# Optimization experiments

Measured on AMD Instinct MI355X. Metric: run time of the kernel, lower is better.

Reference implementation:

```python
import jax, jax.numpy as jnp
import numpy as np

EPS = 1e-5

def _conv(x, w, pad):
    # NCHW conv, stride 1, no bias
    return jax.lax.conv_general_dilated(x, w, (1, 1), [(pad, pad), (pad, pad)],
                                        dimension_numbers=('NCHW', 'OIHW', 'NCHW'))

def _bn(x, g, b, m, v):
    # inference-mode BatchNorm2d folded to scale/shift
    s = g * jax.lax.rsqrt(v + EPS)
    return x * s[None, :, None, None] + (b - m * s)[None, :, None, None]

def _cbr(x, w, g, b, m, v):
    # convolution helper module: 3x3 conv (pad 1, no bias) + BN + ReLU
    return jax.nn.relu(_bn(_conv(x, w, 1), g, b, m, v))


def setup_inputs() -> dict:
    key = jax.random.key(0)
    ks = iter(jax.random.split(key, 40))
    dim, mid, B, H, W = 256, 128, 4, 128, 128
    def conv_w(shape):
        fan = shape[1] * shape[2] * shape[3]
        return jax.random.normal(next(ks), shape, jnp.float32) / np.float32(np.sqrt(fan))
    def bn_p(c):
        return (jax.random.normal(next(ks), (c,), jnp.float32) * 0.1 + 1.0,
                jax.random.normal(next(ks), (c,), jnp.float32) * 0.1,
                jax.random.normal(next(ks), (c,), jnp.float32) * 0.1,
                jax.random.uniform(next(ks), (c,), jnp.float32, 0.5, 1.5))
    x = jax.random.normal(next(ks), (B, dim, H, W), jnp.float32)
    w_p1 = conv_w((mid, dim, 3, 3)); g_p1, b_p1, m_p1, v_p1 = bn_p(mid)
    w_p2 = conv_w((mid, dim, 3, 3)); g_p2, b_p2, m_p2, v_p2 = bn_p(mid)
    w_pc = conv_w((dim, mid, 3, 3)); g_pb, b_pb, m_pb, v_pb = bn_p(dim)
    w_c1 = conv_w((dim, dim, 1, 1)); g_b1, b_b1, m_b1, v_b1 = bn_p(dim)
    w_c2 = conv_w((dim, dim, 3, 3)); g_c2, b_c2, m_c2, v_c2 = bn_p(dim)
    return dict(x=x,
                w_p1=w_p1, g_p1=g_p1, b_p1=b_p1, m_p1=m_p1, v_p1=v_p1,
                w_p2=w_p2, g_p2=g_p2, b_p2=b_p2, m_p2=m_p2, v_p2=v_p2,
                w_pc=w_pc, g_pb=g_pb, b_pb=b_pb, m_pb=m_pb, v_pb=v_pb,
                w_c1=w_c1, g_b1=g_b1, b_b1=b_b1, m_b1=m_b1, v_b1=v_b1,
                w_c2=w_c2, g_c2=g_c2, b_c2=b_c2, m_c2=m_c2, v_c2=v_c2)


def reference(x, w_p1, g_p1, b_p1, m_p1, v_p1,
              w_p2, g_p2, b_p2, m_p2, v_p2,
              w_pc, g_pb, b_pb, m_pb, v_pb,
              w_c1, g_b1, b_b1, m_b1, v_b1,
              w_c2, g_c2, b_c2, m_c2, v_c2):
    p1 = _cbr(x, w_p1, g_p1, b_p1, m_p1, v_p1)          # [B,128,H,W]
    top = jax.lax.cummax(p1, axis=2, reverse=True)       # TopPool: max over rows below
    p2 = _cbr(x, w_p2, g_p2, b_p2, m_p2, v_p2)          # [B,128,H,W]
    left = jax.lax.cummax(p2, axis=3, reverse=True)      # LeftPool: max over cols to the right
    p_bn1 = _bn(_conv(top + left, w_pc, 1), g_pb, b_pb, m_pb, v_pb)  # [B,dim,H,W]
    bn1 = _bn(_conv(x, w_c1, 0), g_b1, b_b1, m_b1, v_b1)             # 1x1 skip branch
    relu1 = jax.nn.relu(p_bn1 + bn1)
    return _cbr(relu1, w_c2, g_c2, b_c2, m_c2, v_c2)
```

## Files before the change

kernel.cpp:

```cpp
#include <hip/hip_runtime.h>
#include <hip/hip_bf16.h>

#define HH 128
#define WW 128
#define BB 4
#define NPIX 16384
#define EPSV 1e-5f

using bfrag = __attribute__((ext_vector_type(8))) short;
using f32x4 = __attribute__((ext_vector_type(4))) float;
using us8   = __attribute__((ext_vector_type(8))) unsigned short;

__device__ __forceinline__ float bf2f(ushort u) {
  union { unsigned int i; float f; } x; x.i = ((unsigned int)u) << 16; return x.f;
}
__device__ __forceinline__ ushort f2bf(float f) {
  union { float f; unsigned int i; } x; x.f = f;
  unsigned int r = x.i + 0x7fffu + ((x.i >> 16) & 1u);
  return (ushort)(r >> 16);
}

#define GLOAD16(gsrc, ldst) \
  __builtin_amdgcn_global_load_lds( \
      (const __attribute__((address_space(1))) unsigned int*)(gsrc), \
      (__attribute__((address_space(3))) unsigned int*)(ldst), 16, 0, 0)

template<int CIN1, int TAPS1, int CIN2, int TAPS2, int EPI>
__global__ __launch_bounds__(256, 2)
void convgemm(const ushort* __restrict__ B1,
              const ushort* __restrict__ B2,
              const ushort* __restrict__ wR,
              const float*  __restrict__ tb,
              const float*  __restrict__ tb2,
              void*          __restrict__ outp,
              const ushort* __restrict__ zerop)
{
  __shared__ ushort lds[2][16384];
  constexpr int nch1 = CIN1 / 64;
  constexpr int nch2 = (CIN2 > 0) ? CIN2 / 64 : 0;
  constexpr int NCH  = TAPS1 * nch1 + TAPS2 * nch2;

  const int g  = blockIdx.x & 7;
  const int r  = blockIdx.x >> 3;
  const int bo = r >> 4;
  const int h  = g * 16 + (r & 15);
  const int o_base = (bo & 1) * 128;
  const int b  = bo >> 1;

  const int tid  = threadIdx.x;
  const int lane = tid & 63;
  const int wid  = tid >> 6;
  const int m0 = (wid >> 1) * 64;
  const int n0 = (wid & 1) * 64;

  f32x4 acc[4][4];
  #pragma unroll
  for (int i = 0; i < 4; ++i)
    #pragma unroll
    for (int j = 0; j < 4; ++j) acc[i][j] = (f32x4){0.f, 0.f, 0.f, 0.f};

  int rowB[4], ro1[4], ro2[4];
  #pragma unroll
  for (int s = 0; s < 4; ++s) {
    const int boff = (wid * 4 + s) * 1024 + lane * 16;
    rowB[s] = boff >> 7;
    const int sl8 = ((((boff >> 4) & 7) ^ (rowB[s] & 7)) << 3);
    ro1[s] = rowB[s] * CIN1 + sl8;
    ro2[s] = (CIN2 > 0) ? rowB[s] * CIN2 + sl8 : 0;
  }
  const size_t B1base = (size_t)b * NPIX * CIN1;
  const size_t B2base = (CIN2 > 0) ? (size_t)b * NPIX * CIN2 : 0;

  auto stage = [&](int t, int buf) {
    char* base = (char*)&lds[buf][0];
    const ushort* wsrc = wR + ((size_t)t * 256 + o_base) * 64;
    const ushort* bch;
    int zr; bool oob, ph2;
    if (CIN2 == 0 || t < TAPS1 * nch1) {
      const int tap = t / nch1, ch = t - tap * nch1;
      const int dy = (TAPS1 == 9) ? tap / 3 - 1 : 0;
      const int dx = (TAPS1 == 9) ? tap - (tap / 3) * 3 - 1 : 0;
      const int hy = h + dy;
      oob = (hy < 0) | (hy >= HH);
      zr  = (dx < 0) ? 0 : ((dx > 0) ? 127 : -1);
      bch = B1 + B1base + (size_t)(hy * WW + dx) * CIN1 + ch * 64;
      ph2 = false;
    } else {
      const int ch = t - TAPS1 * nch1;
      oob = false; zr = -1;
      bch = B2 + B2base + (size_t)(h * WW) * CIN2 + ch * 64;
      ph2 = true;
    }
    #pragma unroll
    for (int s = 0; s < 4; ++s) {
      const int off = (wid * 4 + s) * 1024;
      GLOAD16((const char*)wsrc + off + lane * 16, base + off);
      const int roff = ph2 ? ro2[s] : ro1[s];
      const ushort* bs = (oob || rowB[s] == zr) ? zerop : (bch + roff);
      GLOAD16(bs, base + 16384 + off);
    }
  };

  auto compute = [&](int buf) {
    const char* base = (const char*)&lds[buf][0];
    bfrag af[2][4], bfv[2][4];
    #pragma unroll
    for (int kc = 0; kc < 2; ++kc) {
      const int sw = ((((kc << 2) | (lane >> 4)) ^ (lane & 7)) << 4);
      #pragma unroll
      for (int mf = 0; mf < 4; ++mf)
        af[kc][mf] = *(const bfrag*)(base + (m0 + mf * 16 + (lane & 15)) * 128 + sw);
      #pragma unroll
      for (int nf = 0; nf < 4; ++nf)
        bfv[kc][nf] = *(const bfrag*)(base + 16384 + (n0 + nf * 16 + (lane & 15)) * 128 + sw);
    }
    __builtin_amdgcn_s_setprio(1);
    #pragma unroll
    for (int kc = 0; kc < 2; ++kc)
      #pragma unroll
      for (int mf = 0; mf < 4; ++mf)
        #pragma unroll
        for (int nf = 0; nf < 4; ++nf)
          acc[mf][nf] = __builtin_amdgcn_mfma_f32_16x16x32_bf16(
              af[kc][mf], bfv[kc][nf], acc[mf][nf], 0, 0, 0);
    __builtin_amdgcn_s_setprio(0);
  };

  stage(0, 0);
  int cur = 0;
  for (int t = 0; t < NCH; ++t) {
    asm volatile("s_waitcnt vmcnt(0)" ::: "memory");
    __builtin_amdgcn_s_barrier();
    __builtin_amdgcn_sched_barrier(0);
    if (t + 1 < NCH) stage(t + 1, cur ^ 1);
    compute(cur);
    cur ^= 1;
  }

  if (EPI == 4) {
    __syncthreads();
    ushort* ct = (ushort*)&lds[0][0];
    const int pl0 = n0 + (lane & 15);
    #pragma unroll
    for (int mf = 0; mf < 4; ++mf) {
      #pragma unroll
      for (int r2 = 0; r2 < 4; ++r2) {
        const int ol = m0 + mf * 16 + (lane >> 4) * 4 + r2;
        const int o  = o_base + ol;
        const float bias = tb[o] + tb2[o];
        #pragma unroll
        for (int nf = 0; nf < 4; ++nf)
          ct[(pl0 + nf * 16) * 136 + ol] =
              f2bf(fmaxf(acc[mf][nf][r2] + bias, 0.f));
      }
    }
    __syncthreads();
    const int p  = tid >> 1;
    const int hf = tid & 1;
    ushort* dst = (ushort*)outp +
                  ((size_t)b * NPIX + h * WW + p) * 256 + o_base + hf * 64;
    const ushort* src = ct + p * 136 + hf * 64;
    #pragma unroll
    for (int j = 0; j < 8; ++j)
      *(us8*)(dst + j * 8) = *(const us8*)(src + j * 8);
    return;
  }

  const int pc0 = h * WW + n0 + (lane & 15);
  #pragma unroll
  for (int mf = 0; mf < 4; ++mf) {
    #pragma unroll
    for (int r2 = 0; r2 < 4; ++r2) {
      const int o = o_base + m0 + mf * 16 + (lane >> 4) * 4 + r2;
      const float bias = tb[o];
      #pragma unroll
      for (int nf = 0; nf < 4; ++nf) {
        const int p = pc0 + nf * 16;
        float v = fmaxf(acc[mf][nf][r2] + bias, 0.f);
        const size_t oi = ((size_t)(b * 256 + o)) * NPIX + p;
        if (EPI == 0) ((ushort*)outp)[oi] = f2bf(v);
        else          ((float*)outp)[oi] = v;
      }
    }
  }
}

struct WSeg {
  const float *W, *g, *bb, *mm, *vv;
  ushort* dst; float* tb;
  int CIN, COUT, TAPS, o_off, cb, start, end;
};

__device__ __forceinline__ void wrepack_one(const WSeg& s, int e) {
  const int tap = e % s.TAPS;
  const int ci  = (e / s.TAPS) % s.CIN;
  const int o   = e / (s.TAPS * s.CIN);
  const int oi  = o + s.o_off;
  const float sc = s.g[o] * rsqrtf(s.vv[o] + EPSV);
  const int nch = s.CIN / 64;
  const int ch = ci >> 6, kl = ci & 63;
  const int slot = (kl >> 3) ^ (oi & 7);
  s.dst[(((size_t)((s.cb + tap * nch + ch) * s.COUT) + oi) << 6) +
        (slot << 3) + (kl & 7)] = f2bf(s.W[e] * sc);
  if (ci == 0 && tap == 0) s.tb[oi] = s.bb[o] - s.mm[o] * sc;
}

__global__ __launch_bounds__(256)
void wrepack_all(WSeg s0, WSeg s1, WSeg s2, WSeg s3, WSeg s4) {
  const int id = blockIdx.x * 256 + threadIdx.x;
  if (id < s0.end)      wrepack_one(s0, id - s0.start);
  else if (id < s1.end) wrepack_one(s1, id - s1.start);
  else if (id < s2.end) wrepack_one(s2, id - s2.start);
  else if (id < s3.end) wrepack_one(s3, id - s3.start);
  else if (id < s4.end) wrepack_one(s4, id - s4.start);
}

__global__ __launch_bounds__(256)
void repack_x(const float* __restrict__ x, ushort* __restrict__ xT)
{
  const int b  = blockIdx.z;
  const int cq = threadIdx.x >> 6;
  const int pg = threadIdx.x & 63;
  const int p0 = blockIdx.x * 256 + pg * 4;
  const size_t xb = (size_t)b * 256 * NPIX;
  ushort* ob = xT + ((size_t)b * NPIX + p0) * 256 + cq * 64;
  for (int cc = 0; cc < 64; cc += 8) {
    us8 v[4];
    #pragma unroll
    for (int j = 0; j < 8; ++j) {
      const float4 q = *(const float4*)&x[xb + (size_t)(cq * 64 + cc + j) * NPIX + p0];
      v[0][j] = f2bf(q.x); v[1][j] = f2bf(q.y);
      v[2][j] = f2bf(q.z); v[3][j] = f2bf(q.w);
    }
    #pragma unroll
    for (int k = 0; k < 4; ++k)
      *(us8*)(ob + (size_t)k * 256 + cc) = v[k];
  }
}

__global__ __launch_bounds__(256)
void scan_top(const ushort* __restrict__ p12T, ushort* __restrict__ topT)
{
  const int b = blockIdx.x >> 6;
  const int w = (blockIdx.x & 63) * 2 + (threadIdx.x >> 7);
  const int c = threadIdx.x & 127;
  const size_t ib = (size_t)b * NPIX;
  float cur = -3.4e38f;
  for (int h8 = HH - 8; h8 >= 0; h8 -= 8) {
    float v[8];
    #pragma unroll
    for (int j = 0; j < 8; ++j)
      v[j] = bf2f(p12T[(ib + (size_t)(h8 + j) * WW + w) * 256 + c]);
    #pragma unroll
    for (int j = 7; j >= 0; --j) {
      cur = fmaxf(cur, v[j]);
      topT[(ib + (size_t)(h8 + j) * WW + w) * 128 + c] = f2bf(cur);
    }
  }
}

__global__ __launch_bounds__(256)
void scan_left_sum(const ushort* __restrict__ p12T,
                   const ushort* __restrict__ topT,
                   ushort* __restrict__ sumT)
{
  const int b = blockIdx.x >> 6;
  const int h = (blockIdx.x & 63) * 2 + (threadIdx.x >> 7);
  const int c = threadIdx.x & 127;
  const size_t ib = (size_t)b * NPIX + (size_t)h * WW;
  float cur = -3.4e38f;
  for (int w8 = WW - 8; w8 >= 0; w8 -= 8) {
    float v[8], tv[8];
    #pragma unroll
    for (int j = 0; j < 8; ++j) {
      v[j]  = bf2f(p12T[(ib + w8 + j) * 256 + 128 + c]);
      tv[j] = bf2f(topT[(ib + w8 + j) * 128 + c]);
    }
    #pragma unroll
    for (int j = 7; j >= 0; --j) {
      cur = fmaxf(cur, v[j]);
      sumT[(ib + w8 + j) * 128 + c] = f2bf(cur + tv[j]);
    }
  }
}

extern "C" void kernel_launch(void* const* d_in, const int* in_sizes, int n_in,
                              void* d_out, int out_size, void* d_ws, size_t ws_size,
                              hipStream_t stream) {
  const float* x    = (const float*)d_in[0];
  const float* w_p1 = (const float*)d_in[1];
  const float* g_p1 = (const float*)d_in[2];
  const float* b_p1 = (const float*)d_in[3];
  const float* m_p1 = (const float*)d_in[4];
  const float* v_p1 = (const float*)d_in[5];
  const float* w_p2 = (const float*)d_in[6];
  const float* g_p2 = (const float*)d_in[7];
  const float* b_p2 = (const float*)d_in[8];
  const float* m_p2 = (const float*)d_in[9];
  const float* v_p2 = (const float*)d_in[10];
  const float* w_pc = (const float*)d_in[11];
  const float* g_pb = (const float*)d_in[12];
  const float* b_pb = (const float*)d_in[13];
  const float* m_pb = (const float*)d_in[14];
  const float* v_pb = (const float*)d_in[15];
  const float* w_c1 = (const float*)d_in[16];
  const float* g_b1 = (const float*)d_in[17];
  const float* b_b1 = (const float*)d_in[18];
  const float* m_b1 = (const float*)d_in[19];
  const float* v_b1 = (const float*)d_in[20];
  const float* w_c2 = (const float*)d_in[21];
  const float* g_c2 = (const float*)d_in[22];
  const float* b_c2 = (const float*)d_in[23];
  const float* m_c2 = (const float*)d_in[24];
  const float* v_c2 = (const float*)d_in[25];

  char* ws = (char*)d_ws;
  ushort* xT      = (ushort*)(ws + 0);
  ushort* p12T    = (ushort*)(ws + 33554432);
  ushort* relu1T  = (ushort*)(ws + 33554432);
  ushort* sumT    = (ushort*)(ws + 67108864);
  ushort* topT    = (ushort*)(ws + 83886080);
  ushort* wR_p12  = (ushort*)(ws + 100663296);
  ushort* wR_pcc1 = (ushort*)(ws + 101842944);
  ushort* wR_c2   = (ushort*)(ws + 102563840);
  float*  tb_p12  = (float*)(ws + 103743488);
  float*  tb_pc   = (float*)(ws + 103744512);
  float*  tb_c1   = (float*)(ws + 103745536);
  float*  tb_c2   = (float*)(ws + 103746560);
  ushort* zerop   = (ushort*)(ws + 103747584);
  float*  tb_zero = (float*)(ws + 103747840);

  hipMemsetAsync(zerop, 0, 256 + 1024, stream);

  const int n_p  = 128 * 256 * 9;
  const int n_pc = 256 * 128 * 9;
  const int n_c1 = 256 * 256 * 1;
  const int n_c2 = 256 * 256 * 9;
  WSeg s0 = {w_p1, g_p1, b_p1, m_p1, v_p1, wR_p12, tb_p12, 256, 256, 9, 0, 0,
             0, n_p};
  WSeg s1 = {w_p2, g_p2, b_p2, m_p2, v_p2, wR_p12, tb_p12, 256, 256, 9, 128, 0,
             n_p, 2 * n_p};
  WSeg s2 = {w_pc, g_pb, b_pb, m_pb, v_pb, wR_pcc1, tb_pc, 128, 256, 9, 0, 0,
             2 * n_p, 2 * n_p + n_pc};
  WSeg s3 = {w_c1, g_b1, b_b1, m_b1, v_b1, wR_pcc1, tb_c1, 256, 256, 1, 0, 18,
             2 * n_p + n_pc, 2 * n_p + n_pc + n_c1};
  WSeg s4 = {w_c2, g_c2, b_c2, m_c2, v_c2, wR_c2, tb_c2, 256, 256, 9, 0, 0,
             2 * n_p + n_pc + n_c1, 2 * n_p + n_pc + n_c1 + n_c2};
  const int n_all = 2 * n_p + n_pc + n_c1 + n_c2;
  wrepack_all<<<dim3((n_all + 255) / 256), 256, 0, stream>>>(s0, s1, s2, s3, s4);

  repack_x<<<dim3(NPIX / 256, 1, BB), 256, 0, stream>>>(x, xT);

  convgemm<256, 9, 0, 0, 4><<<dim3(1024), 256, 0, stream>>>(
      xT, nullptr, wR_p12, tb_p12, tb_zero, p12T, zerop);

  scan_top<<<dim3(BB * 64), 256, 0, stream>>>(p12T, topT);
  scan_left_sum<<<dim3(BB * 64), 256, 0, stream>>>(p12T, topT, sumT);

  convgemm<128, 9, 256, 1, 4><<<dim3(1024), 256, 0, stream>>>(
      sumT, xT, wR_pcc1, tb_pc, tb_c1, relu1T, zerop);

  convgemm<256, 9, 0, 0, 3><<<dim3(1024), 256, 0, stream>>>(
      relu1T, nullptr, wR_c2, tb_c2, nullptr, (void*)d_out, zerop);
}
```

Measured before the change: 288.6 us.

## Enlarge conv GEMM tile to 256 outputs by 256 pixels with 512-thread blocks

Each conv GEMM block now covers all 256 output channels and two image rows (256 pixels) using 8 waves and 128 KB of double-buffered LDS, instead of a 128x128 tile with 4 waves. Each staged weight and activation chunk is reused across twice as many MFMAs, which cuts global and LDS traffic per FLOP. MFMAs are interleaved with the fragment LDS reads. The cost is only 256 blocks, one per CU, with 128 accumulator registers per thread, which lowers occupancy and leaves less latency hiding on MI355X's 256 CUs.

```diff
diff --git a/kernel.cpp b/kernel.cpp
--- a/kernel.cpp
+++ b/kernel.cpp
@@ -26,7 +26,7 @@
       (__attribute__((address_space(3))) unsigned int*)(ldst), 16, 0, 0)
 
 template<int CIN1, int TAPS1, int CIN2, int TAPS2, int EPI>
-__global__ __launch_bounds__(256, 2)
+__global__ __launch_bounds__(512, 1)
 void convgemm(const ushort* __restrict__ B1,
               const ushort* __restrict__ B2,
               const ushort* __restrict__ wR,
@@ -35,149 +35,170 @@
               void*          __restrict__ outp,
               const ushort* __restrict__ zerop)
 {
-  __shared__ ushort lds[2][16384];
+  __shared__ char ldsb[131072];
   constexpr int nch1 = CIN1 / 64;
   constexpr int nch2 = (CIN2 > 0) ? CIN2 / 64 : 0;
   constexpr int NCH  = TAPS1 * nch1 + TAPS2 * nch2;
 
-  const int g  = blockIdx.x & 7;
-  const int r  = blockIdx.x >> 3;
-  const int bo = r >> 4;
-  const int h  = g * 16 + (r & 15);
-  const int o_base = (bo & 1) * 128;
-  const int b  = bo >> 1;
+  const int nid = (blockIdx.x & 7) * 32 + (blockIdx.x >> 3);
+  const int b   = nid >> 6;
+  const int h2  = (nid & 63) * 2;
 
   const int tid  = threadIdx.x;
   const int lane = tid & 63;
   const int wid  = tid >> 6;
-  const int m0 = (wid >> 1) * 64;
-  const int n0 = (wid & 1) * 64;
-
-  f32x4 acc[4][4];
+  const int wc   = wid & 3;
+  const int m0   = (wid >> 2) * 128;
+  const int n0   = wc * 64;
+
+  f32x4 acc[8][4];
   #pragma unroll
-  for (int i = 0; i < 4; ++i)
+  for (int i = 0; i < 8; ++i)
     #pragma unroll
     for (int j = 0; j < 4; ++j) acc[i][j] = (f32x4){0.f, 0.f, 0.f, 0.f};
 
-  int rowB[4], ro1[4], ro2[4];
+  const int sl8 = (((tid & 7) ^ ((tid >> 3) & 7)) << 3);
+  int ro1[4], ro2[4], w_[4], prow_[4];
   #pragma unroll
   for (int s = 0; s < 4; ++s) {
-    const int boff = (wid * 4 + s) * 1024 + lane * 16;
-    rowB[s] = boff >> 7;
-    const int sl8 = ((((boff >> 4) & 7) ^ (rowB[s] & 7)) << 3);
-    ro1[s] = rowB[s] * CIN1 + sl8;
-    ro2[s] = (CIN2 > 0) ? rowB[s] * CIN2 + sl8 : 0;
+    const int rowB = s * 64 + (tid >> 3);
+    prow_[s] = rowB >> 7;
+    w_[s]    = rowB & 127;
+    ro1[s]   = (prow_[s] * WW + w_[s]) * CIN1 + sl8;
+    ro2[s]   = (CIN2 > 0) ? rowB * CIN2 + sl8 : 0;
   }
   const size_t B1base = (size_t)b * NPIX * CIN1;
   const size_t B2base = (CIN2 > 0) ? (size_t)b * NPIX * CIN2 : 0;
 
   auto stage = [&](int t, int buf) {
-    char* base = (char*)&lds[buf][0];
-    const ushort* wsrc = wR + ((size_t)t * 256 + o_base) * 64;
-    const ushort* bch;
-    int zr; bool oob, ph2;
+    char* baseA = ldsb + buf * 65536;
+    char* baseB = baseA + 32768;
     if (CIN2 == 0 || t < TAPS1 * nch1) {
       const int tap = t / nch1, ch = t - tap * nch1;
       const int dy = (TAPS1 == 9) ? tap / 3 - 1 : 0;
       const int dx = (TAPS1 == 9) ? tap - (tap / 3) * 3 - 1 : 0;
-      const int hy = h + dy;
-      oob = (hy < 0) | (hy >= HH);
-      zr  = (dx < 0) ? 0 : ((dx > 0) ? 127 : -1);
-      bch = B1 + B1base + (size_t)(hy * WW + dx) * CIN1 + ch * 64;
-      ph2 = false;
+      const int hy0 = h2 + dy;
+      const bool oob0 = (hy0 < 0) | (hy0 > 127);
+      const bool oob1 = (hy0 + 1 < 0) | (hy0 + 1 > 127);
+      const int zr = (dx < 0) ? 0 : ((dx > 0) ? 127 : -1);
+      const ushort* bch = B1 + B1base + (size_t)(hy0 * WW + dx) * CIN1 + ch * 64;
+      #pragma unroll
+      for (int s = 0; s < 4; ++s) {
+        const bool bad = (prow_[s] ? oob1 : oob0) || (w_[s] == zr);
+        const ushort* src = bad ? zerop : (bch + ro1[s]);
+        GLOAD16(src, baseB + s * 8192 + tid * 16);
+      }
     } else {
       const int ch = t - TAPS1 * nch1;
-      oob = false; zr = -1;
-      bch = B2 + B2base + (size_t)(h * WW) * CIN2 + ch * 64;
-      ph2 = true;
-    }
-    #pragma unroll
-    for (int s = 0; s < 4; ++s) {
-      const int off = (wid * 4 + s) * 1024;
-      GLOAD16((const char*)wsrc + off + lane * 16, base + off);
-      const int roff = ph2 ? ro2[s] : ro1[s];
-      const ushort* bs = (oob || rowB[s] == zr) ? zerop : (bch + roff);
-      GLOAD16(bs, base + 16384 + off);
-    }
+      const ushort* bch = B2 + B2base + (size_t)(h2 * WW) * CIN2 + ch * 64;
+      #pragma unroll
+      for (int s = 0; s < 4; ++s)
+        GLOAD16(bch + ro2[s], baseB + s * 8192 + tid * 16);
+    }
+    const char* wsrc = (const char*)(wR + (size_t)t * (256 * 64));
+    #pragma unroll
+    for (int i = 0; i < 4; ++i)
+      GLOAD16(wsrc + i * 8192 + tid * 16, baseA + i * 8192 + tid * 16);
   };
 
-  auto compute = [&](int buf) {
-    const char* base = (const char*)&lds[buf][0];
-    bfrag af[2][4], bfv[2][4];
-    #pragma unroll
-    for (int kc = 0; kc < 2; ++kc) {
-      const int sw = ((((kc << 2) | (lane >> 4)) ^ (lane & 7)) << 4);
-      #pragma unroll
-      for (int mf = 0; mf < 4; ++mf)
-        af[kc][mf] = *(const bfrag*)(base + (m0 + mf * 16 + (lane & 15)) * 128 + sw);
-      #pragma unroll
-      for (int nf = 0; nf < 4; ++nf)
-        bfv[kc][nf] = *(const bfrag*)(base + 16384 + (n0 + nf * 16 + (lane & 15)) * 128 + sw);
-    }
-    __builtin_amdgcn_s_setprio(1);
-    #pragma unroll
-    for (int kc = 0; kc < 2; ++kc)
-      #pragma unroll
-      for (int mf = 0; mf < 4; ++mf)
-        #pragma unroll
-        for (int nf = 0; nf < 4; ++nf)
-          acc[mf][nf] = __builtin_amdgcn_mfma_f32_16x16x32_bf16(
-              af[kc][mf], bfv[kc][nf], acc[mf][nf], 0, 0, 0);
-    __builtin_amdgcn_s_setprio(0);
-  };
+#define READ_A(dst_, mfh_, kc_) do { \
+    const int sw_ = ((((kc_) << 2) | (lane >> 4)) ^ (lane & 7)) << 4; \
+    _Pragma("unroll") \
+    for (int mf_ = 0; mf_ < 4; ++mf_) \
+      dst_[mf_] = *(const bfrag*)(cb + \
+          (m0 + (mfh_) * 64 + mf_ * 16 + (lane & 15)) * 128 + sw_); \
+  } while (0)
+
+#define READ_B(dst_, kc_) do { \
+    const int sw_ = ((((kc_) << 2) | (lane >> 4)) ^ (lane & 7)) << 4; \
+    _Pragma("unroll") \
+    for (int nf_ = 0; nf_ < 4; ++nf_) \
+      dst_[nf_] = *(const bfrag*)(cb + 32768 + \
+          (n0 + nf_ * 16 + (lane & 15)) * 128 + sw_); \
+  } while (0)
+
+#define MFMA16(rb_, A_, B_) do { \
+    __builtin_amdgcn_s_setprio(1); \
+    _Pragma("unroll") \
+    for (int mf_ = 0; mf_ < 4; ++mf_) \
+      _Pragma("unroll") \
+      for (int nf_ = 0; nf_ < 4; ++nf_) \
+        acc[(rb_) + mf_][nf_] = __builtin_amdgcn_mfma_f32_16x16x32_bf16( \
+            A_[mf_], B_[nf_], acc[(rb_) + mf_][nf_], 0, 0, 0); \
+    __builtin_amdgcn_s_setprio(0); \
+  } while (0)
 
   stage(0, 0);
-  int cur = 0;
   for (int t = 0; t < NCH; ++t) {
     asm volatile("s_waitcnt vmcnt(0)" ::: "memory");
     __builtin_amdgcn_s_barrier();
     __builtin_amdgcn_sched_barrier(0);
-    if (t + 1 < NCH) stage(t + 1, cur ^ 1);
-    compute(cur);
-    cur ^= 1;
-  }
+    if (t + 1 < NCH) stage(t + 1, (t + 1) & 1);
+    __builtin_amdgcn_sched_barrier(0);
+    const char* cb = ldsb + (t & 1) * 65536;
+    bfrag B0[4], B1f[4], A00[4], A10[4], A01[4], A11[4];
+    READ_B(B0, 0);
+    READ_A(A00, 0, 0);
+    MFMA16(0, A00, B0);
+    READ_A(A10, 1, 0);
+    MFMA16(4, A10, B0);
+    READ_B(B1f, 1);
+    READ_A(A01, 0, 1);
+    MFMA16(0, A01, B1f);
+    READ_A(A11, 1, 1);
+    MFMA16(4, A11, B1f);
+  }
+#undef READ_A
+#undef READ_B
+#undef MFMA16
 
   if (EPI == 4) {
-    __syncthreads();
-    ushort* ct = (ushort*)&lds[0][0];
-    const int pl0 = n0 + (lane & 15);
-    #pragma unroll
-    for (int mf = 0; mf < 4; ++mf) {
+    ushort* ct = (ushort*)ldsb;
+    #pragma unroll
+    for (int ph = 0; ph < 2; ++ph) {
+      __syncthreads();
+      if ((wc >> 1) == ph) {
+        const int lp0 = (wc & 1) * 64 + (lane & 15);
+        #pragma unroll
+        for (int mf = 0; mf < 8; ++mf) {
+          #pragma unroll
+          for (int r2 = 0; r2 < 4; ++r2) {
+            const int o = m0 + mf * 16 + (lane >> 4) * 4 + r2;
+            const float bias = tb[o] + tb2[o];
+            #pragma unroll
+            for (int nf = 0; nf < 4; ++nf)
+              ct[(lp0 + nf * 16) * 264 + o] =
+                  f2bf(fmaxf(acc[mf][nf][r2] + bias, 0.f));
+          }
+        }
+      }
+      __syncthreads();
+      const int lp = tid >> 2;
+      const int q  = tid & 3;
+      ushort* dst = (ushort*)outp +
+          ((size_t)b * NPIX + (h2 + ph) * WW + lp) * 256 + q * 64;
+      const ushort* src = ct + lp * 264 + q * 64;
       #pragma unroll
-      for (int r2 = 0; r2 < 4; ++r2) {
-        const int ol = m0 + mf * 16 + (lane >> 4) * 4 + r2;
-        const int o  = o_base + ol;
-        const float bias = tb[o] + tb2[o];
-        #pragma unroll
-        for (int nf = 0; nf < 4; ++nf)
-          ct[(pl0 + nf * 16) * 136 + ol] =
-              f2bf(fmaxf(acc[mf][nf][r2] + bias, 0.f));
-      }
-    }
-    __syncthreads();
-    const int p  = tid >> 1;
-    const int hf = tid & 1;
-    ushort* dst = (ushort*)outp +
-                  ((size_t)b * NPIX + h * WW + p) * 256 + o_base + hf * 64;
-    const ushort* src = ct + p * 136 + hf * 64;
-    #pragma unroll
-    for (int j = 0; j < 8; ++j)
-      *(us8*)(dst + j * 8) = *(const us8*)(src + j * 8);
+      for (int j = 0; j < 8; ++j)
+        *(us8*)(dst + j * 8) = *(const us8*)(src + j * 8);
+    }
     return;
   }
 
-  const int pc0 = h * WW + n0 + (lane & 15);
+  const int prow = wc >> 1;
+  const int hout = h2 + prow;
+  const int wbase = (wc & 1) * 64 + (lane & 15);
   #pragma unroll
-  for (int mf = 0; mf < 4; ++mf) {
+  for (int mf = 0; mf < 8; ++mf) {
     #pragma unroll
     for (int r2 = 0; r2 < 4; ++r2) {
-      const int o = o_base + m0 + mf * 16 + (lane >> 4) * 4 + r2;
+      const int o = m0 + mf * 16 + (lane >> 4) * 4 + r2;
       const float bias = tb[o];
       #pragma unroll
       for (int nf = 0; nf < 4; ++nf) {
-        const int p = pc0 + nf * 16;
+        const int w = wbase + nf * 16;
         float v = fmaxf(acc[mf][nf][r2] + bias, 0.f);
-        const size_t oi = ((size_t)(b * 256 + o)) * NPIX + p;
+        const size_t oi = (((size_t)(b * 256 + o)) << 14) + hout * WW + w;
         if (EPI == 0) ((ushort*)outp)[oi] = f2bf(v);
         else          ((float*)outp)[oi] = v;
       }
@@ -351,15 +372,15 @@
 
   repack_x<<<dim3(NPIX / 256, 1, BB), 256, 0, stream>>>(x, xT);
 
-  convgemm<256, 9, 0, 0, 4><<<dim3(1024), 256, 0, stream>>>(
+  convgemm<256, 9, 0, 0, 4><<<dim3(256), 512, 0, stream>>>(
       xT, nullptr, wR_p12, tb_p12, tb_zero, p12T, zerop);
 
   scan_top<<<dim3(BB * 64), 256, 0, stream>>>(p12T, topT);
   scan_left_sum<<<dim3(BB * 64), 256, 0, stream>>>(p12T, topT, sumT);
 
-  convgemm<128, 9, 256, 1, 4><<<dim3(1024), 256, 0, stream>>>(
+  convgemm<128, 9, 256, 1, 4><<<dim3(256), 512, 0, stream>>>(
       sumT, xT, wR_pcc1, tb_pc, tb_c1, relu1T, zerop);
 
-  convgemm<256, 9, 0, 0, 3><<<dim3(1024), 256, 0, stream>>>(
+  convgemm<256, 9, 0, 0, 3><<<dim3(256), 512, 0, stream>>>(
       relu1T, nullptr, wR_c2, tb_c2, nullptr, (void*)d_out, zerop);
 }
```

Measured after the change: 281.5 us. 1.03x faster.

## Reuse staged input row across the three horizontal conv taps

Applied to the files above, without the earlier changes.

The implicit-GEMM conv kernel now stages each input row (per dy and channel chunk) once into LDS with a one-pixel zero halo on each side. The three dx taps then read that same buffer at shifted row offsets instead of reloading it, which cuts global-to-LDS activation traffic for 3x3 convs to about a third. The cost is a larger LDS footprint (about 66KB), which may lower occupancy below the declared two blocks per CU. It also adds shifted-swizzle addressing and a buffer-parity scheme that reuses B buffers across consecutive iterations.

```diff
diff --git a/kernel.cpp b/kernel.cpp
--- a/kernel.cpp
+++ b/kernel.cpp
@@ -35,15 +35,17 @@
               void*          __restrict__ outp,
               const ushort* __restrict__ zerop)
 {
-  __shared__ ushort lds[2][16384];
+  __shared__ char ldsbuf[66048];
   constexpr int nch1 = CIN1 / 64;
   constexpr int nch2 = (CIN2 > 0) ? CIN2 / 64 : 0;
-  constexpr int NCH  = TAPS1 * nch1 + TAPS2 * nch2;
-
-  const int g  = blockIdx.x & 7;
+  constexpr int NG1  = 3 * nch1;
+  constexpr int NT1  = 9 * nch1;
+  constexpr int NT   = NT1 + nch2;
+
+  const int gx = blockIdx.x & 7;
   const int r  = blockIdx.x >> 3;
   const int bo = r >> 4;
-  const int h  = g * 16 + (r & 15);
+  const int h  = gx * 16 + (r & 15);
   const int o_base = (bo & 1) * 128;
   const int b  = bo >> 1;
 
@@ -59,60 +61,97 @@
     #pragma unroll
     for (int j = 0; j < 4; ++j) acc[i][j] = (f32x4){0.f, 0.f, 0.f, 0.f};
 
-  int rowB[4], ro1[4], ro2[4];
+  int ro1[4], ro2[4];
   #pragma unroll
   for (int s = 0; s < 4; ++s) {
     const int boff = (wid * 4 + s) * 1024 + lane * 16;
-    rowB[s] = boff >> 7;
-    const int sl8 = ((((boff >> 4) & 7) ^ (rowB[s] & 7)) << 3);
-    ro1[s] = rowB[s] * CIN1 + sl8;
-    ro2[s] = (CIN2 > 0) ? rowB[s] * CIN2 + sl8 : 0;
+    const int p    = boff >> 7;
+    const int koff = ((((boff >> 4) & 7) ^ ((p + 1) & 7)) << 3);
+    ro1[s] = p * CIN1 + koff;
+    ro2[s] = (CIN2 > 0) ? p * CIN2 + koff : 0;
   }
   const size_t B1base = (size_t)b * NPIX * CIN1;
   const size_t B2base = (CIN2 > 0) ? (size_t)b * NPIX * CIN2 : 0;
 
-  auto stage = [&](int t, int buf) {
-    char* base = (char*)&lds[buf][0];
-    const ushort* wsrc = wR + ((size_t)t * 256 + o_base) * 64;
-    const ushort* bch;
-    int zr; bool oob, ph2;
-    if (CIN2 == 0 || t < TAPS1 * nch1) {
-      const int tap = t / nch1, ch = t - tap * nch1;
-      const int dy = (TAPS1 == 9) ? tap / 3 - 1 : 0;
-      const int dx = (TAPS1 == 9) ? tap - (tap / 3) * 3 - 1 : 0;
-      const int hy = h + dy;
-      oob = (hy < 0) | (hy >= HH);
-      zr  = (dx < 0) ? 0 : ((dx > 0) ? 127 : -1);
-      bch = B1 + B1base + (size_t)(hy * WW + dx) * CIN1 + ch * 64;
-      ph2 = false;
+  auto stageA = [&](int tA, int buf) {
+    char* dst = ldsbuf + buf * 16384;
+    const char* wsrc = (const char*)(wR + ((size_t)tA * 256 + o_base) * 64);
+    #pragma unroll
+    for (int s = 0; s < 4; ++s)
+      GLOAD16(wsrc + s * 4096 + tid * 16, dst + s * 4096 + tid * 16);
+  };
+
+  auto stageB = [&](int gg, int buf) {
+    char* dst = ldsbuf + 32768 + buf * 16640 + 128;
+    if (CIN2 == 0 || gg < NG1) {
+      const int dy = gg / nch1, ch = gg - dy * nch1;
+      const int hy = h + dy - 1;
+      const bool oob = (hy < 0) | (hy >= HH);
+      const ushort* bch = B1 + B1base + (size_t)(hy * WW) * CIN1 + ch * 64;
+      #pragma unroll
+      for (int s = 0; s < 4; ++s) {
+        const ushort* src = oob ? zerop : (bch + ro1[s]);
+        GLOAD16(src, dst + (wid * 4 + s) * 1024 + lane * 16);
+      }
     } else {
-      const int ch = t - TAPS1 * nch1;
-      oob = false; zr = -1;
-      bch = B2 + B2base + (size_t)(h * WW) * CIN2 + ch * 64;
-      ph2 = true;
-    }
-    #pragma unroll
-    for (int s = 0; s < 4; ++s) {
-      const int off = (wid * 4 + s) * 1024;
-      GLOAD16((const char*)wsrc + off + lane * 16, base + off);
-      const int roff = ph2 ? ro2[s] : ro1[s];
-      const ushort* bs = (oob || rowB[s] == zr) ? zerop : (bch + roff);
-      GLOAD16(bs, base + 16384 + off);
+      const int ch = gg - NG1;
+      const ushort* bch = B2 + B2base + (size_t)(h * WW) * CIN2 + ch * 64;
+      #pragma unroll
+      for (int s = 0; s < 4; ++s)
+        GLOAD16(bch + ro2[s], dst + (wid * 4 + s) * 1024 + lane * 16);
     }
   };
 
-  auto compute = [&](int buf) {
-    const char* base = (const char*)&lds[buf][0];
+  auto g_of = [&](int i) -> int {
+    return (CIN2 == 0 || i < NT1) ? i / 3 : NG1 + (i - NT1);
+  };
+  auto tA_of = [&](int i) -> int {
+    if (CIN2 == 0 || i < NT1) {
+      const int gg = i / 3, dxi = i - gg * 3;
+      const int dy = gg / nch1, ch = gg - dy * nch1;
+      return (dy * 3 + dxi) * nch1 + ch;
+    }
+    return i;
+  };
+
+  if (tid < 32) {
+    const int buf = tid >> 4;
+    const int k   = tid & 15;
+    const int row = (k >> 3) ? 129 : 0;
+    char* hz = ldsbuf + 32768 + buf * 16640 + row * 128 + (k & 7) * 16;
+    us8 z = (us8){0,0,0,0,0,0,0,0};
+    *(us8*)hz = z;
+  }
+  __syncthreads();
+
+  stageB(0, 0);
+  stageA(tA_of(0), 0);
+  for (int i = 0; i < NT; ++i) {
+    asm volatile("s_waitcnt vmcnt(0)" ::: "memory");
+    __builtin_amdgcn_s_barrier();
+    __builtin_amdgcn_sched_barrier(0);
+    const int gg = g_of(i);
+    const int dx = (CIN2 == 0 || i < NT1) ? (i - (i / 3) * 3) - 1 : 0;
+    if (i + 1 < NT) {
+      stageA(tA_of(i + 1), (i + 1) & 1);
+      const int gn = g_of(i + 1);
+      if (gn != gg) stageB(gn, gn & 1);
+    }
+    const char* Ab = ldsbuf + (i & 1) * 16384;
+    const char* Bb = ldsbuf + 32768 + (gg & 1) * 16640;
     bfrag af[2][4], bfv[2][4];
     #pragma unroll
     for (int kc = 0; kc < 2; ++kc) {
-      const int sw = ((((kc << 2) | (lane >> 4)) ^ (lane & 7)) << 4);
+      const int swa = ((((kc << 2) | (lane >> 4)) ^ (lane & 7)) << 4);
       #pragma unroll
       for (int mf = 0; mf < 4; ++mf)
-        af[kc][mf] = *(const bfrag*)(base + (m0 + mf * 16 + (lane & 15)) * 128 + sw);
-      #pragma unroll
-      for (int nf = 0; nf < 4; ++nf)
-        bfv[kc][nf] = *(const bfrag*)(base + 16384 + (n0 + nf * 16 + (lane & 15)) * 128 + sw);
+        af[kc][mf] = *(const bfrag*)(Ab + (m0 + mf * 16 + (lane & 15)) * 128 + swa);
+      #pragma unroll
+      for (int nf = 0; nf < 4; ++nf) {
+        const int row = n0 + nf * 16 + (lane & 15) + 1 + dx;
+        const int swb = ((((kc << 2) | (lane >> 4)) ^ (row & 7)) << 4);
+        bfv[kc][nf] = *(const bfrag*)(Bb + row * 128 + swb);
+      }
     }
     __builtin_amdgcn_s_setprio(1);
     #pragma unroll
@@ -124,22 +163,11 @@
           acc[mf][nf] = __builtin_amdgcn_mfma_f32_16x16x32_bf16(
               af[kc][mf], bfv[kc][nf], acc[mf][nf], 0, 0, 0);
     __builtin_amdgcn_s_setprio(0);
-  };
-
-  stage(0, 0);
-  int cur = 0;
-  for (int t = 0; t < NCH; ++t) {
-    asm volatile("s_waitcnt vmcnt(0)" ::: "memory");
-    __builtin_amdgcn_s_barrier();
-    __builtin_amdgcn_sched_barrier(0);
-    if (t + 1 < NCH) stage(t + 1, cur ^ 1);
-    compute(cur);
-    cur ^= 1;
   }
 
   if (EPI == 4) {
     __syncthreads();
-    ushort* ct = (ushort*)&lds[0][0];
+    ushort* ct = (ushort*)ldsbuf;
     const int pl0 = n0 + (lane & 15);
     #pragma unroll
     for (int mf = 0; mf < 4; ++mf) {
```

New measurement: 268.1 us. -7.1%, faster.
